# Performance work log

Measured on AMD Instinct MI355X. Metric: run time of the kernel, lower is better.

The kernel has to match this reference:

```python
import jax, jax.numpy as jnp
import numpy as np

N_TOKENS = 4096
EMBED = 1024
ATTN = 64


def setup_inputs() -> dict:
    key = jax.random.key(0)
    k1, k2, k3, k4 = jax.random.split(key, 4)
    tokens = jax.random.normal(k1, (N_TOKENS, EMBED), dtype=jnp.float32)
    mask = jnp.ones((1, N_TOKENS), dtype=jnp.float32)
    W_Q = jax.random.uniform(k2, (EMBED, ATTN), dtype=jnp.float32)
    W_K = jax.random.uniform(k3, (EMBED, ATTN), dtype=jnp.float32)
    W_V = jax.random.uniform(k4, (EMBED, ATTN), dtype=jnp.float32)
    return {"tokens": tokens, "mask": mask, "W_Q": W_Q, "W_K": W_K, "W_V": W_V}


def reference(tokens, mask, W_Q, W_K, W_V):
    # Q, K, V: (n_tokens, attn)
    Q = tokens @ W_Q
    K = tokens @ W_K
    V = tokens @ W_V
    scale = jnp.sqrt(jnp.asarray(ATTN, dtype=tokens.dtype))
    # scores: (n_tokens, n_tokens); multiplicative mask then scale, as in source
    scores = (Q @ K.T) * mask
    attn = jax.nn.softmax(scores / scale, axis=1)
    return attn @ V
```

## Files before the change

kernel.cpp:

```cpp
#include <hip/hip_runtime.h>
#include <math.h>

#define NT 4096
#define EMB 1024
#define DH 64
#define PLANE (NT * DH)
#define NSPLIT 16
#define KPS (NT / NSPLIT)
#define KVB 64
#define KSPLIT 8

typedef __attribute__((ext_vector_type(8))) short short8;
typedef __attribute__((ext_vector_type(16))) float f32x16;
typedef unsigned short u16;

union U8 { short8 s; uint4 u; unsigned short h[8]; unsigned int w[4]; };

static __device__ __forceinline__ unsigned short f2bf(float x) {
    union { float f; unsigned int u; } v; v.f = x;
    unsigned int r = v.u + 0x7fffu + ((v.u >> 16) & 1u);
    return (unsigned short)(r >> 16);
}
static __device__ __forceinline__ float bf2f(unsigned short h) {
    union { unsigned int u; float f; } v; v.u = ((unsigned int)h) << 16;
    return v.f;
}
static __device__ __forceinline__ unsigned int pk2(float a, float b) {
    return (unsigned int)f2bf(a) | ((unsigned int)f2bf(b) << 16);
}

__global__ __launch_bounds__(256) void prep_w(
    const float* __restrict__ wq, const float* __restrict__ wk,
    const float* __restrict__ wv,
    u16* __restrict__ WtSh, u16* __restrict__ WtSl)
{
    int tid = blockIdx.x * 256 + threadIdx.x;
    int col = tid >> 7;
    int ch  = tid & 127;
    const float* W = (col < 64) ? wq : (col < 128) ? wk : wv;
    int wcol = col & 63;
    int k0 = ch * 8;
    U8 H, L;
#pragma unroll
    for (int i = 0; i < 8; ++i) {
        float x = W[(size_t)(k0 + i) * DH + wcol];
        H.h[i] = f2bf(x);
        L.h[i] = f2bf(x - bf2f(H.h[i]));
    }
    *(uint4*)&WtSh[(size_t)col * EMB + k0] = H.u;
    *(uint4*)&WtSl[(size_t)col * EMB + k0] = L.u;
}

__global__ __launch_bounds__(256) void proj_mfma(
    const float* __restrict__ tokens,
    const u16* __restrict__ WtSh, const u16* __restrict__ WtSl,
    float* __restrict__ part)
{
    __shared__ u16 Th[128][64];
    __shared__ u16 Tl[128][64];
    __shared__ u16 Wh[96][64];
    __shared__ u16 Wl[96][64];

    const int t  = threadIdx.x;
    const int rb = blockIdx.x;
    const int cb = blockIdx.y;
    const int ks = blockIdx.z;
    const int w    = t >> 6;
    const int lane = t & 63;
    const int g    = lane >> 5;
    const int c    = lane & 31;
    const int rowbase = rb * 128;

    f32x16 acc[3];
#pragma unroll
    for (int ct = 0; ct < 3; ++ct)
#pragma unroll
        for (int i = 0; i < 16; ++i) acc[ct][i] = 0.f;

    for (int st = 0; st < 2; ++st) {
        const int kbase = ks * (EMB / KSPLIT) + st * 64;
        __syncthreads();
#pragma unroll
        for (int i = 0; i < 4; ++i) {
            int idx = t + 256 * i;
            int r = idx >> 3;
            int slot = idx & 7;
            const float* gp = tokens + (size_t)(rowbase + r) * EMB + kbase + slot * 8;
            float4 a = *(const float4*)gp;
            float4 b = *(const float4*)(gp + 4);
            float x[8] = {a.x, a.y, a.z, a.w, b.x, b.y, b.z, b.w};
            U8 H, L;
#pragma unroll
            for (int j = 0; j < 8; ++j) {
                H.h[j] = f2bf(x[j]);
                L.h[j] = f2bf(x[j] - bf2f(H.h[j]));
            }
            int dst = (slot ^ (r & 7)) * 8;
            *(uint4*)&Th[r][dst] = H.u;
            *(uint4*)&Tl[r][dst] = L.u;
        }
#pragma unroll
        for (int i = 0; i < 3; ++i) {
            int idx = t + 256 * i;
            int r = idx >> 3;
            int slot = idx & 7;
            size_t gidx = (size_t)(cb * 96 + r) * EMB + kbase + slot * 8;
            uint4 h = *(const uint4*)&WtSh[gidx];
            uint4 l = *(const uint4*)&WtSl[gidx];
            int dst = (slot ^ (r & 7)) * 8;
            *(uint4*)&Wh[r][dst] = h;
            *(uint4*)&Wl[r][dst] = l;
        }
        __syncthreads();

#pragma unroll
        for (int kt = 0; kt < 4; ++kt) {
            int sA = kt * 2 + g;
            int offA = ((sA ^ (c & 7)) * 8);
            short8 ah = *(const short8*)&Th[w * 32 + c][offA];
            short8 al = *(const short8*)&Tl[w * 32 + c][offA];
#pragma unroll
            for (int ct = 0; ct < 3; ++ct) {
                short8 bh = *(const short8*)&Wh[ct * 32 + c][offA];
                short8 bl = *(const short8*)&Wl[ct * 32 + c][offA];
                acc[ct] = __builtin_amdgcn_mfma_f32_32x32x16_bf16(ah, bh, acc[ct], 0, 0, 0);
                acc[ct] = __builtin_amdgcn_mfma_f32_32x32x16_bf16(ah, bl, acc[ct], 0, 0, 0);
                acc[ct] = __builtin_amdgcn_mfma_f32_32x32x16_bf16(al, bh, acc[ct], 0, 0, 0);
            }
        }
    }

#pragma unroll
    for (int ct = 0; ct < 3; ++ct)
#pragma unroll
        for (int r = 0; r < 16; ++r) {
            int row_l = (r & 3) + 8 * (r >> 2) + 4 * g;
            part[((size_t)ks * NT + rowbase + w * 32 + row_l) * 192 + cb * 96 + ct * 32 + c]
                = acc[ct][r];
        }
}

__global__ __launch_bounds__(256) void merge_conv(
    const float* __restrict__ part, const float* __restrict__ mask,
    u16* __restrict__ Qhg, u16* __restrict__ Qlg,
    u16* __restrict__ Khg, u16* __restrict__ Klg, u16* __restrict__ Vbg)
{
    int tid = blockIdx.x * 256 + threadIdx.x;
    int row = tid / 24;
    int c8  = tid % 24;
    int colbase = c8 * 8;

    float v[8];
#pragma unroll
    for (int i = 0; i < 8; ++i) v[i] = 0.f;
#pragma unroll
    for (int s = 0; s < KSPLIT; ++s) {
        const float* p = part + ((size_t)s * NT + row) * 192 + colbase;
        float4 a = *(const float4*)p;
        float4 b = *(const float4*)(p + 4);
        v[0] += a.x; v[1] += a.y; v[2] += a.z; v[3] += a.w;
        v[4] += b.x; v[5] += b.y; v[6] += b.z; v[7] += b.w;
    }

    int plane = colbase >> 6;
    int pc = colbase & 63;
    size_t o = (size_t)row * DH + pc;
    if (plane == 0) {
        U8 H, L;
#pragma unroll
        for (int i = 0; i < 8; ++i) {
            H.h[i] = f2bf(v[i]);
            L.h[i] = f2bf(v[i] - bf2f(H.h[i]));
        }
        *(uint4*)&Qhg[o] = H.u;
        *(uint4*)&Qlg[o] = L.u;
    } else if (plane == 1) {
        float mk = mask[row] * 0.125f;
        U8 H, L;
#pragma unroll
        for (int i = 0; i < 8; ++i) {
            float x = v[i] * mk;
            H.h[i] = f2bf(x);
            L.h[i] = f2bf(x - bf2f(H.h[i]));
        }
        *(uint4*)&Khg[o] = H.u;
        *(uint4*)&Klg[o] = L.u;
    } else {
        U8 H;
#pragma unroll
        for (int i = 0; i < 8; ++i) H.h[i] = f2bf(v[i]);
        *(uint4*)&Vbg[o] = H.u;
    }
}

__global__ __launch_bounds__(256) void attn_mfma(
    const u16* __restrict__ Qhg, const u16* __restrict__ Qlg,
    const u16* __restrict__ Khg, const u16* __restrict__ Klg,
    const u16* __restrict__ Vbg,
    float* __restrict__ opart, float* __restrict__ mlbuf)
{
    __shared__ u16 Kh[64][64];
    __shared__ u16 Kl[64][64];
    __shared__ unsigned int V2[32][64];

    const int t    = threadIdx.x;
    const int qb   = blockIdx.x;
    const int sp   = blockIdx.y;
    const int wq   = t >> 6;
    const int lane = t & 63;
    const int g    = lane >> 5;
    const int c    = lane & 31;
    const int qrow = qb * 128 + wq * 32 + c;

    short8 qh[4], ql[4];
#pragma unroll
    for (int kt = 0; kt < 4; ++kt) {
        size_t o = (size_t)qrow * DH + kt * 16 + g * 8;
        U8 H, L;
        H.u = *(const uint4*)&Qhg[o];
        L.u = *(const uint4*)&Qlg[o];
        qh[kt] = H.s;
        ql[kt] = L.s;
    }

    f32x16 oa[2];
#pragma unroll
    for (int i = 0; i < 16; ++i) { oa[0][i] = 0.f; oa[1][i] = 0.f; }
    float m = -INFINITY, l = 0.f;

    for (int cb = 0; cb < KPS / KVB; ++cb) {
        const int kv = sp * KPS + cb * KVB;
        __syncthreads();
#pragma unroll
        for (int it = 0; it < 2; ++it) {
            int idx = it * 256 + t;
            int j = idx >> 3, gr = idx & 7;
            int colp = (gr * 8) ^ ((j & 7) * 8);
            *(uint4*)&Kh[j][colp] = *(const uint4*)&Khg[(size_t)(kv + j) * DH + gr * 8];
            *(uint4*)&Kl[j][colp] = *(const uint4*)&Klg[(size_t)(kv + j) * DH + gr * 8];
        }
        {
            int a2 = t >> 3, dg = t & 7;
            uint4 r0 = *(const uint4*)&Vbg[(size_t)(kv + a2 * 2) * DH + dg * 8];
            uint4 r1 = *(const uint4*)&Vbg[(size_t)(kv + a2 * 2 + 1) * DH + dg * 8];
            const unsigned int* p0 = (const unsigned int*)&r0;
            const unsigned int* p1 = (const unsigned int*)&r1;
            unsigned int wv_[8];
#pragma unroll
            for (int i = 0; i < 4; ++i) {
                wv_[2 * i]     = (p0[i] & 0xFFFFu) | (p1[i] << 16);
                wv_[2 * i + 1] = (p0[i] >> 16)     | (p1[i] & 0xFFFF0000u);
            }
            int colp = (dg * 8) ^ ((a2 & 7) * 8);
            *(uint4*)&V2[a2][colp]     = *(uint4*)&wv_[0];
            *(uint4*)&V2[a2][colp + 4] = *(uint4*)&wv_[4];
        }
        __syncthreads();

        f32x16 st0, st1;
#pragma unroll
        for (int i = 0; i < 16; ++i) { st0[i] = 0.f; st1[i] = 0.f; }
#pragma unroll
        for (int kt = 0; kt < 4; ++kt) {
            int colp = ((kt * 2 + g) * 8) ^ ((c & 7) * 8);
            short8 kh0 = *(const short8*)&Kh[c][colp];
            short8 kl0 = *(const short8*)&Kl[c][colp];
            short8 kh1 = *(const short8*)&Kh[32 + c][colp];
            short8 kl1 = *(const short8*)&Kl[32 + c][colp];
            st0 = __builtin_amdgcn_mfma_f32_32x32x16_bf16(kh0, qh[kt], st0, 0, 0, 0);
            st1 = __builtin_amdgcn_mfma_f32_32x32x16_bf16(kh1, qh[kt], st1, 0, 0, 0);
            st0 = __builtin_amdgcn_mfma_f32_32x32x16_bf16(kh0, ql[kt], st0, 0, 0, 0);
            st1 = __builtin_amdgcn_mfma_f32_32x32x16_bf16(kh1, ql[kt], st1, 0, 0, 0);
            st0 = __builtin_amdgcn_mfma_f32_32x32x16_bf16(kl0, qh[kt], st0, 0, 0, 0);
            st1 = __builtin_amdgcn_mfma_f32_32x32x16_bf16(kl1, qh[kt], st1, 0, 0, 0);
        }

        float p[32];
        float pm = -INFINITY;
#pragma unroll
        for (int r = 0; r < 16; ++r) {
            pm = fmaxf(pm, st0[r]);
            pm = fmaxf(pm, st1[r]);
        }
        pm = fmaxf(pm, __shfl_xor(pm, 32));
        float mn = fmaxf(m, pm);
        float f  = __expf(m - mn);
        float rs = 0.f;
#pragma unroll
        for (int r = 0; r < 16; ++r) { p[r]      = __expf(st0[r] - mn); rs += p[r]; }
#pragma unroll
        for (int r = 0; r < 16; ++r) { p[16 + r] = __expf(st1[r] - mn); rs += p[16 + r]; }
        rs += __shfl_xor(rs, 32);
        l = l * f + rs;
        m = mn;

        short8 pa[4];
#pragma unroll
        for (int jt = 0; jt < 2; ++jt) {
            const float* pp = &p[jt * 16];
            unsigned int A1 = pk2(pp[0], pp[1]),   B1 = pk2(pp[4], pp[5]);
            unsigned int A2 = pk2(pp[2], pp[3]),   B2 = pk2(pp[6], pp[7]);
            unsigned int A3 = pk2(pp[8], pp[9]),   B3 = pk2(pp[12], pp[13]);
            unsigned int A4 = pk2(pp[10], pp[11]), B4 = pk2(pp[14], pp[15]);
            unsigned int xA1 = (unsigned int)__shfl_xor((int)A1, 32);
            unsigned int xB1 = (unsigned int)__shfl_xor((int)B1, 32);
            unsigned int xA2 = (unsigned int)__shfl_xor((int)A2, 32);
            unsigned int xB2 = (unsigned int)__shfl_xor((int)B2, 32);
            unsigned int xA3 = (unsigned int)__shfl_xor((int)A3, 32);
            unsigned int xB3 = (unsigned int)__shfl_xor((int)B3, 32);
            unsigned int xA4 = (unsigned int)__shfl_xor((int)A4, 32);
            unsigned int xB4 = (unsigned int)__shfl_xor((int)B4, 32);
            U8 f0, f1;
            f0.w[0] = g ? xB1 : A1;
            f0.w[1] = g ? xB2 : A2;
            f0.w[2] = g ? B1  : xA1;
            f0.w[3] = g ? B2  : xA2;
            f1.w[0] = g ? xB3 : A3;
            f1.w[1] = g ? xB4 : A4;
            f1.w[2] = g ? B3  : xA3;
            f1.w[3] = g ? B4  : xA4;
            pa[jt * 2]     = f0.s;
            pa[jt * 2 + 1] = f1.s;
        }

#pragma unroll
        for (int r = 0; r < 16; ++r) {
            float fr = __shfl(f, (r & 3) + 8 * (r >> 2) + 4 * g);
            oa[0][r] *= fr;
            oa[1][r] *= fr;
        }

#pragma unroll
        for (int dt = 0; dt < 2; ++dt) {
#pragma unroll
            for (int ksl = 0; ksl < 4; ++ksl) {
                U8 bf;
#pragma unroll
                for (int pq = 0; pq < 4; ++pq) {
                    int j2 = ksl * 8 + g * 4 + pq;
                    int col = (dt * 32 + c) ^ ((j2 & 7) * 8);
                    bf.w[pq] = V2[j2][col];
                }
                oa[dt] = __builtin_amdgcn_mfma_f32_32x32x16_bf16(pa[ksl], bf.s, oa[dt], 0, 0, 0);
            }
        }
    }

#pragma unroll
    for (int dt = 0; dt < 2; ++dt)
#pragma unroll
        for (int r = 0; r < 16; ++r) {
            int row = qb * 128 + wq * 32 + ((r & 3) + 8 * (r >> 2) + 4 * g);
            opart[((size_t)sp * NT + row) * DH + dt * 32 + c] = oa[dt][r];
        }
    if (lane < 32) {
        int row = qb * 128 + wq * 32 + lane;
        mlbuf[((size_t)sp * NT + row) * 2 + 0] = m;
        mlbuf[((size_t)sp * NT + row) * 2 + 1] = l;
    }
}

__global__ __launch_bounds__(256) void merge_kernel(
    const float* __restrict__ opart, const float* __restrict__ mlbuf,
    float* __restrict__ out)
{
    int idx = (blockIdx.x * 256 + threadIdx.x) * 4;
    int row = idx >> 6;
    int d0  = idx & 63;

    float mv[NSPLIT], lv[NSPLIT];
    float mstar = -INFINITY;
#pragma unroll
    for (int s = 0; s < NSPLIT; ++s) {
        mv[s] = mlbuf[((size_t)s * NT + row) * 2 + 0];
        lv[s] = mlbuf[((size_t)s * NT + row) * 2 + 1];
        mstar = fmaxf(mstar, mv[s]);
    }
    float denom = 0.f;
    float ax = 0.f, ay = 0.f, az = 0.f, aw = 0.f;
#pragma unroll
    for (int s = 0; s < NSPLIT; ++s) {
        float w = __expf(mv[s] - mstar);
        denom += w * lv[s];
        float4 ov = *(const float4*)&opart[((size_t)s * NT + row) * DH + d0];
        ax += w * ov.x; ay += w * ov.y; az += w * ov.z; aw += w * ov.w;
    }
    float inv = 1.f / denom;
    *(float4*)&out[idx] = make_float4(ax * inv, ay * inv, az * inv, aw * inv);
}

extern "C" void kernel_launch(void* const* d_in, const int* in_sizes, int n_in,
                              void* d_out, int out_size, void* d_ws, size_t ws_size,
                              hipStream_t stream) {
    const float* tokens = (const float*)d_in[0];
    const float* mask   = (const float*)d_in[1];
    const float* wq     = (const float*)d_in[2];
    const float* wk     = (const float*)d_in[3];
    const float* wv     = (const float*)d_in[4];

    char* wsb = (char*)d_ws;
    u16* WtSh = (u16*)wsb;
    u16* WtSl = WtSh + 192 * EMB;
    u16* Qhg  = WtSl + 192 * EMB;
    u16* Qlg  = Qhg + PLANE;
    u16* Khg  = Qlg + PLANE;
    u16* Klg  = Khg + PLANE;
    u16* Vbg  = Klg + PLANE;
    float* window = (float*)(Vbg + PLANE);
    float* part   = window;
    float* opart  = window;
    float* mlbuf  = window + (size_t)NSPLIT * PLANE;
    float* out    = (float*)d_out;

    hipLaunchKernelGGL(prep_w, dim3(96), dim3(256), 0, stream,
                       wq, wk, wv, WtSh, WtSl);
    hipLaunchKernelGGL(proj_mfma, dim3(32, 2, KSPLIT), dim3(256), 0, stream,
                       tokens, WtSh, WtSl, part);
    hipLaunchKernelGGL(merge_conv, dim3(384), dim3(256), 0, stream,
                       part, mask, Qhg, Qlg, Khg, Klg, Vbg);
    hipLaunchKernelGGL(attn_mfma, dim3(NT / 128, NSPLIT), dim3(256), 0, stream,
                       Qhg, Qlg, Khg, Klg, Vbg, opart, mlbuf);
    hipLaunchKernelGGL(merge_kernel, dim3(256), dim3(256), 0, stream,
                       opart, mlbuf, out);
}
```

Measured before the change: 53.83 us.

## Use packed bf16 converts, exp2 softmax, and bf16 normalized attention partials

Replaces the manual round-to-nearest bf16 conversions with the hardware v_cvt_pk_bf16_f32 instruction throughout. It folds log2(e) into the K scaling so the softmax can use exp2f. The attention kernel now normalizes each split's output by its own l and stores the partials as bf16, which halves the partial-output traffic, and the merge is adjusted to weight by l·exp2. The bf16 partials reduce precision of the intermediate outputs, and the workspace offsets are now hardcoded.

Result: faster. 50.88 us (-5.5%).

```diff
diff --git a/kernel.cpp b/kernel.cpp
--- a/kernel.cpp
+++ b/kernel.cpp
@@ -9,6 +9,7 @@
 #define KPS (NT / NSPLIT)
 #define KVB 64
 #define KSPLIT 8
+#define LOG2E 1.44269504088896f
 
 typedef __attribute__((ext_vector_type(8))) short short8;
 typedef __attribute__((ext_vector_type(16))) float f32x16;
@@ -25,8 +26,18 @@
     union { unsigned int u; float f; } v; v.u = ((unsigned int)h) << 16;
     return v.f;
 }
-static __device__ __forceinline__ unsigned int pk2(float a, float b) {
-    return (unsigned int)f2bf(a) | ((unsigned int)f2bf(b) << 16);
+static __device__ __forceinline__ unsigned int cvtpk(float a, float b) {
+    unsigned int r;
+    asm("v_cvt_pk_bf16_f32 %0, %1, %2" : "=v"(r) : "v"(a), "v"(b));
+    return r;
+}
+static __device__ __forceinline__ void split2(float a, float b,
+                                              unsigned int& h, unsigned int& lo) {
+    h = cvtpk(a, b);
+    union { unsigned int u; float f; } ua, ub;
+    ua.u = h << 16;
+    ub.u = h & 0xffff0000u;
+    lo = cvtpk(a - ua.f, b - ub.f);
 }
 
 __global__ __launch_bounds__(256) void prep_w(
@@ -40,15 +51,16 @@
     const float* W = (col < 64) ? wq : (col < 128) ? wk : wv;
     int wcol = col & 63;
     int k0 = ch * 8;
-    U8 H, L;
-#pragma unroll
-    for (int i = 0; i < 8; ++i) {
-        float x = W[(size_t)(k0 + i) * DH + wcol];
-        H.h[i] = f2bf(x);
-        L.h[i] = f2bf(x - bf2f(H.h[i]));
-    }
-    *(uint4*)&WtSh[(size_t)col * EMB + k0] = H.u;
-    *(uint4*)&WtSl[(size_t)col * EMB + k0] = L.u;
+    float x[8];
+#pragma unroll
+    for (int i = 0; i < 8; ++i) x[i] = W[(size_t)(k0 + i) * DH + wcol];
+    uint4 H, L;
+    split2(x[0], x[1], H.x, L.x);
+    split2(x[2], x[3], H.y, L.y);
+    split2(x[4], x[5], H.z, L.z);
+    split2(x[6], x[7], H.w, L.w);
+    *(uint4*)&WtSh[(size_t)col * EMB + k0] = H;
+    *(uint4*)&WtSl[(size_t)col * EMB + k0] = L;
 }
 
 __global__ __launch_bounds__(256) void proj_mfma(
@@ -88,28 +100,24 @@
             const float* gp = tokens + (size_t)(rowbase + r) * EMB + kbase + slot * 8;
             float4 a = *(const float4*)gp;
             float4 b = *(const float4*)(gp + 4);
-            float x[8] = {a.x, a.y, a.z, a.w, b.x, b.y, b.z, b.w};
-            U8 H, L;
-#pragma unroll
-            for (int j = 0; j < 8; ++j) {
-                H.h[j] = f2bf(x[j]);
-                L.h[j] = f2bf(x[j] - bf2f(H.h[j]));
-            }
+            uint4 H, L;
+            split2(a.x, a.y, H.x, L.x);
+            split2(a.z, a.w, H.y, L.y);
+            split2(b.x, b.y, H.z, L.z);
+            split2(b.z, b.w, H.w, L.w);
             int dst = (slot ^ (r & 7)) * 8;
-            *(uint4*)&Th[r][dst] = H.u;
-            *(uint4*)&Tl[r][dst] = L.u;
+            *(uint4*)&Th[r][dst] = H;
+            *(uint4*)&Tl[r][dst] = L;
         }
 #pragma unroll
         for (int i = 0; i < 3; ++i) {
             int idx = t + 256 * i;
             int r = idx >> 3;
             int slot = idx & 7;
-            size_t gidx = (size_t)(cb * 96 + r) * EMB + kbase + slot * 8;
-            uint4 h = *(const uint4*)&WtSh[gidx];
-            uint4 l = *(const uint4*)&WtSl[gidx];
+            size_t gi = (size_t)(cb * 96 + r) * EMB + kbase + slot * 8;
             int dst = (slot ^ (r & 7)) * 8;
-            *(uint4*)&Wh[r][dst] = h;
-            *(uint4*)&Wl[r][dst] = l;
+            *(uint4*)&Wh[r][dst] = *(const uint4*)&WtSh[gi];
+            *(uint4*)&Wl[r][dst] = *(const uint4*)&WtSl[gi];
         }
         __syncthreads();
 
@@ -166,30 +174,29 @@
     int pc = colbase & 63;
     size_t o = (size_t)row * DH + pc;
     if (plane == 0) {
-        U8 H, L;
-#pragma unroll
-        for (int i = 0; i < 8; ++i) {
-            H.h[i] = f2bf(v[i]);
-            L.h[i] = f2bf(v[i] - bf2f(H.h[i]));
-        }
-        *(uint4*)&Qhg[o] = H.u;
-        *(uint4*)&Qlg[o] = L.u;
+        uint4 H, L;
+        split2(v[0], v[1], H.x, L.x);
+        split2(v[2], v[3], H.y, L.y);
+        split2(v[4], v[5], H.z, L.z);
+        split2(v[6], v[7], H.w, L.w);
+        *(uint4*)&Qhg[o] = H;
+        *(uint4*)&Qlg[o] = L;
     } else if (plane == 1) {
-        float mk = mask[row] * 0.125f;
-        U8 H, L;
-#pragma unroll
-        for (int i = 0; i < 8; ++i) {
-            float x = v[i] * mk;
-            H.h[i] = f2bf(x);
-            L.h[i] = f2bf(x - bf2f(H.h[i]));
-        }
-        *(uint4*)&Khg[o] = H.u;
-        *(uint4*)&Klg[o] = L.u;
+        float mk = mask[row] * 0.125f * LOG2E;
+        uint4 H, L;
+        split2(v[0] * mk, v[1] * mk, H.x, L.x);
+        split2(v[2] * mk, v[3] * mk, H.y, L.y);
+        split2(v[4] * mk, v[5] * mk, H.z, L.z);
+        split2(v[6] * mk, v[7] * mk, H.w, L.w);
+        *(uint4*)&Khg[o] = H;
+        *(uint4*)&Klg[o] = L;
     } else {
-        U8 H;
-#pragma unroll
-        for (int i = 0; i < 8; ++i) H.h[i] = f2bf(v[i]);
-        *(uint4*)&Vbg[o] = H.u;
+        uint4 H;
+        H.x = cvtpk(v[0], v[1]);
+        H.y = cvtpk(v[2], v[3]);
+        H.z = cvtpk(v[4], v[5]);
+        H.w = cvtpk(v[6], v[7]);
+        *(uint4*)&Vbg[o] = H;
     }
 }
 
@@ -197,7 +204,7 @@
     const u16* __restrict__ Qhg, const u16* __restrict__ Qlg,
     const u16* __restrict__ Khg, const u16* __restrict__ Klg,
     const u16* __restrict__ Vbg,
-    float* __restrict__ opart, float* __restrict__ mlbuf)
+    u16* __restrict__ opart, float* __restrict__ mlbuf)
 {
     __shared__ u16 Kh[64][64];
     __shared__ u16 Kl[64][64];
@@ -284,12 +291,12 @@
         }
         pm = fmaxf(pm, __shfl_xor(pm, 32));
         float mn = fmaxf(m, pm);
-        float f  = __expf(m - mn);
+        float f  = exp2f(m - mn);
         float rs = 0.f;
 #pragma unroll
-        for (int r = 0; r < 16; ++r) { p[r]      = __expf(st0[r] - mn); rs += p[r]; }
-#pragma unroll
-        for (int r = 0; r < 16; ++r) { p[16 + r] = __expf(st1[r] - mn); rs += p[16 + r]; }
+        for (int r = 0; r < 16; ++r) { p[r]      = exp2f(st0[r] - mn); rs += p[r]; }
+#pragma unroll
+        for (int r = 0; r < 16; ++r) { p[16 + r] = exp2f(st1[r] - mn); rs += p[16 + r]; }
         rs += __shfl_xor(rs, 32);
         l = l * f + rs;
         m = mn;
@@ -298,10 +305,10 @@
 #pragma unroll
         for (int jt = 0; jt < 2; ++jt) {
             const float* pp = &p[jt * 16];
-            unsigned int A1 = pk2(pp[0], pp[1]),   B1 = pk2(pp[4], pp[5]);
-            unsigned int A2 = pk2(pp[2], pp[3]),   B2 = pk2(pp[6], pp[7]);
-            unsigned int A3 = pk2(pp[8], pp[9]),   B3 = pk2(pp[12], pp[13]);
-            unsigned int A4 = pk2(pp[10], pp[11]), B4 = pk2(pp[14], pp[15]);
+            unsigned int A1 = cvtpk(pp[0], pp[1]),   B1 = cvtpk(pp[4], pp[5]);
+            unsigned int A2 = cvtpk(pp[2], pp[3]),   B2 = cvtpk(pp[6], pp[7]);
+            unsigned int A3 = cvtpk(pp[8], pp[9]),   B3 = cvtpk(pp[12], pp[13]);
+            unsigned int A4 = cvtpk(pp[10], pp[11]), B4 = cvtpk(pp[14], pp[15]);
             unsigned int xA1 = (unsigned int)__shfl_xor((int)A1, 32);
             unsigned int xB1 = (unsigned int)__shfl_xor((int)B1, 32);
             unsigned int xA2 = (unsigned int)__shfl_xor((int)A2, 32);
@@ -346,13 +353,16 @@
         }
     }
 
-#pragma unroll
-    for (int dt = 0; dt < 2; ++dt)
-#pragma unroll
-        for (int r = 0; r < 16; ++r) {
-            int row = qb * 128 + wq * 32 + ((r & 3) + 8 * (r >> 2) + 4 * g);
-            opart[((size_t)sp * NT + row) * DH + dt * 32 + c] = oa[dt][r];
-        }
+    float inv = 1.f / l;
+#pragma unroll
+    for (int r = 0; r < 16; ++r) {
+        int crow = (r & 3) + 8 * (r >> 2) + 4 * g;
+        float li = __shfl(inv, crow);
+        int row = qb * 128 + wq * 32 + crow;
+        size_t o = ((size_t)sp * NT + row) * DH + c;
+        opart[o]      = f2bf(oa[0][r] * li);
+        opart[o + 32] = f2bf(oa[1][r] * li);
+    }
     if (lane < 32) {
         int row = qb * 128 + wq * 32 + lane;
         mlbuf[((size_t)sp * NT + row) * 2 + 0] = m;
@@ -361,7 +371,7 @@
 }
 
 __global__ __launch_bounds__(256) void merge_kernel(
-    const float* __restrict__ opart, const float* __restrict__ mlbuf,
+    const u16* __restrict__ opart, const float* __restrict__ mlbuf,
     float* __restrict__ out)
 {
     int idx = (blockIdx.x * 256 + threadIdx.x) * 4;
@@ -380,10 +390,13 @@
     float ax = 0.f, ay = 0.f, az = 0.f, aw = 0.f;
 #pragma unroll
     for (int s = 0; s < NSPLIT; ++s) {
-        float w = __expf(mv[s] - mstar);
-        denom += w * lv[s];
-        float4 ov = *(const float4*)&opart[((size_t)s * NT + row) * DH + d0];
-        ax += w * ov.x; ay += w * ov.y; az += w * ov.z; aw += w * ov.w;
+        float w = lv[s] * exp2f(mv[s] - mstar);
+        denom += w;
+        uint2 ov = *(const uint2*)&opart[((size_t)s * NT + row) * DH + d0];
+        ax += w * bf2f((u16)(ov.x & 0xFFFFu));
+        ay += w * bf2f((u16)(ov.x >> 16));
+        az += w * bf2f((u16)(ov.y & 0xFFFFu));
+        aw += w * bf2f((u16)(ov.y >> 16));
     }
     float inv = 1.f / denom;
     *(float4*)&out[idx] = make_float4(ax * inv, ay * inv, az * inv, aw * inv);
@@ -397,8 +410,9 @@
     const float* wq     = (const float*)d_in[2];
     const float* wk     = (const float*)d_in[3];
     const float* wv     = (const float*)d_in[4];
-
-    char* wsb = (char*)d_ws;
+    char*  wsb = (char*)d_ws;
+    float* out = (float*)d_out;
+
     u16* WtSh = (u16*)wsb;
     u16* WtSl = WtSh + 192 * EMB;
     u16* Qhg  = WtSl + 192 * EMB;
@@ -406,11 +420,9 @@
     u16* Khg  = Qlg + PLANE;
     u16* Klg  = Khg + PLANE;
     u16* Vbg  = Klg + PLANE;
-    float* window = (float*)(Vbg + PLANE);
-    float* part   = window;
-    float* opart  = window;
-    float* mlbuf  = window + (size_t)NSPLIT * PLANE;
-    float* out    = (float*)d_out;
+    float* part  = (float*)(wsb + (size_t)4 * 1024 * 1024);
+    u16*   opart = (u16*)(wsb + (size_t)4 * 1024 * 1024);
+    float* mlbuf = (float*)(wsb + (size_t)28 * 1024 * 1024);
 
     hipLaunchKernelGGL(prep_w, dim3(96), dim3(256), 0, stream,
                        wq, wk, wv, WtSh, WtSl);
```
